# Kernel optimization log

Hardware: AMD Instinct MI355X
Metric: run time of the kernel (lower is better)

## Reference

```python
import jax, jax.numpy as jnp
import numpy as np

N_NODES = 100000
N_EDGES = 3200000
N_GRAPHS = 1000
IN_DIM = 10
HID = 20
N_CLASSES = 2
BN_EPS = 1e-5


def setup_inputs() -> dict:
    key = jax.random.key(0)
    ks = jax.random.split(key, 12)
    x = jax.random.normal(ks[0], (N_NODES, IN_DIM), dtype=jnp.float32)
    edge_index = jax.random.randint(ks[1], (2, N_EDGES), 0, N_NODES, dtype=jnp.int64)
    batch = jnp.sort(jax.random.randint(ks[2], (N_NODES,), 0, N_GRAPHS, dtype=jnp.int64))
    def lin(k, fan_in, fan_out):
        bound = 1.0 / np.sqrt(fan_in)
        kw, kb = jax.random.split(k)
        W = jax.random.uniform(kw, (fan_in, fan_out), jnp.float32, -bound, bound)
        b = jax.random.uniform(kb, (fan_out,), jnp.float32, -bound, bound)
        return W, b
    W1, b1 = lin(ks[3], IN_DIM, HID)
    W2, b2 = lin(ks[4], HID, HID)
    W3, b3 = lin(ks[5], HID, HID)
    fcW, fcb = lin(ks[6], HID, N_CLASSES)
    ones = jnp.ones((HID,), jnp.float32)
    zeros = jnp.zeros((HID,), jnp.float32)
    return {
        "x": x, "edge_index": edge_index, "batch": batch,
        "W1": W1, "b1": b1, "g1": ones, "beta1": zeros,
        "W2": W2, "b2": b2, "g2": ones, "beta2": zeros,
        "W3": W3, "b3": b3, "g3": ones, "beta3": zeros,
        "fcW": fcW, "fcb": fcb,
    }


def _gin_layer(h, src, dst, W, b, g, beta):
    # GIN aggregation: (1+eps)*x_i + sum_{j->i} x_j, eps = 0
    agg = jax.ops.segment_sum(h[src], dst, num_segments=N_NODES)  # [N, d]
    h = (h + agg) @ W + b                                          # MLP (single Linear)
    mu = jnp.mean(h, axis=0)                                       # BatchNorm (batch stats)
    var = jnp.mean(jnp.square(h - mu), axis=0)
    h = (h - mu) * jax.lax.rsqrt(var + BN_EPS) * g + beta
    return jax.nn.relu(h)                                          # dropout p=0 is identity


def reference(x, edge_index, batch, W1, b1, g1, beta1, W2, b2, g2, beta2,
              W3, b3, g3, beta3, fcW, fcb):
    src, dst = edge_index[0], edge_index[1]
    h = _gin_layer(x, src, dst, W1, b1, g1, beta1)
    h = _gin_layer(h, src, dst, W2, b2, g2, beta2)
    h = _gin_layer(h, src, dst, W3, b3, g3, beta3)
    graph_emb = jax.ops.segment_sum(h, batch, num_segments=N_GRAPHS)  # global add pool
    return graph_emb @ fcW + fcb
```

## Files before the change

### kernel.cpp

```cpp
#include <hip/hip_runtime.h>
#include <hip/hip_bf16.h>

#define N_NODES  100000
#define N_EDGES  3200000
#define N_GRAPHS 1000
#define IN_DIM   10
#define HID      20
#define BN_EPS   1e-5f

#define BSH   7
#define NB    ((N_NODES + 127) / 128)
#define FILL_BLOCKS 512
#define CHUNK ((N_EDGES + FILL_BLOCKS - 1) / FILL_BLOCKS)
#define MAXB  6144
#define NBG   ((N_NODES + 31) / 32)

__global__ __launch_bounds__(256) void hist_bucket(const int* __restrict__ dst,
                                                   int* __restrict__ gcnt) {
    __shared__ int cnt[NB];
    for (int i = threadIdx.x; i < NB; i += 256) cnt[i] = 0;
    __syncthreads();
    int e0 = blockIdx.x * CHUNK;
    int e1 = min(e0 + CHUNK, N_EDGES);
    for (int e = e0 + threadIdx.x; e < e1; e += 256)
        atomicAdd(&cnt[dst[e] >> BSH], 1);
    __syncthreads();
    for (int i = threadIdx.x; i < NB; i += 256)
        if (cnt[i]) atomicAdd(&gcnt[i], cnt[i]);
}

__global__ void scan_buckets(const int* __restrict__ gcnt,
                             int* __restrict__ off, int* __restrict__ cursor) {
    __shared__ int lds[1024];
    int t = threadIdx.x;
    int v = (t < NB) ? gcnt[t] : 0;
    int val = v;
    lds[t] = val; __syncthreads();
    for (int o = 1; o < 1024; o <<= 1) {
        int a = (t >= o) ? lds[t - o] : 0;
        __syncthreads();
        val += a; lds[t] = val;
        __syncthreads();
    }
    if (t < NB) { off[t] = val - v; cursor[t] = val - v; }
    if (t == 0) off[NB] = N_EDGES;
}

__global__ __launch_bounds__(256) void fill_bucket(const int* __restrict__ src,
                                                   const int* __restrict__ dst,
                                                   int* __restrict__ cursor,
                                                   unsigned* __restrict__ packed) {
    __shared__ int cnt[NB];
    __shared__ int base[NB];
    for (int i = threadIdx.x; i < NB; i += 256) cnt[i] = 0;
    __syncthreads();
    int e0 = blockIdx.x * CHUNK;
    int e1 = min(e0 + CHUNK, N_EDGES);
    for (int e = e0 + threadIdx.x; e < e1; e += 256)
        atomicAdd(&cnt[dst[e] >> BSH], 1);
    __syncthreads();
    for (int i = threadIdx.x; i < NB; i += 256) {
        int c = cnt[i];
        base[i] = c ? atomicAdd(&cursor[i], c) : 0;
        cnt[i] = 0;
    }
    __syncthreads();
    for (int e = e0 + threadIdx.x; e < e1; e += 256) {
        int d = dst[e];
        int b = d >> BSH;
        int lr = atomicAdd(&cnt[b], 1);
        packed[base[b] + lr] = (unsigned)src[e] | ((unsigned)(d & 127) << 24);
    }
}

__global__ __launch_bounds__(256) void sort_bucket(const unsigned* __restrict__ packed,
                                                   const int* __restrict__ off,
                                                   int* __restrict__ csr,
                                                   int* __restrict__ rp) {
    __shared__ unsigned ebuf[MAXB];
    __shared__ int cnt[256];
    __shared__ int cur[256];
    int b = blockIdx.x, t = threadIdx.x;
    int e0 = off[b], e1 = off[b + 1], m = e1 - e0;
    bool inl = (m <= MAXB);
    if (inl)
        for (int i = t; i < m; i += 256) ebuf[i] = packed[e0 + i];
    cnt[t] = 0;
    __syncthreads();
    for (int i = t; i < m; i += 256) {
        unsigned p = inl ? ebuf[i] : packed[e0 + i];
        atomicAdd(&cnt[p >> 24], 1);
    }
    __syncthreads();
    int v = cnt[t], val = v;
    cur[t] = val; __syncthreads();
    for (int o = 1; o < 256; o <<= 1) {
        int a = (t >= o) ? cur[t - o] : 0;
        __syncthreads();
        val += a; cur[t] = val;
        __syncthreads();
    }
    int excl = val - v;
    if (t < 128) {
        int node = b * 128 + t;
        if (node <= N_NODES) rp[node] = e0 + excl;
    }
    cur[t] = excl;
    __syncthreads();
    for (int i = t; i < m; i += 256) {
        unsigned p = inl ? ebuf[i] : packed[e0 + i];
        int l = p >> 24;
        int pos = atomicAdd(&cur[l], 1);
        csr[e0 + pos] = (int)(p & 0xFFFFFFu);
    }
}

template<int DIN, bool BN>
__global__ __launch_bounds__(256) void gather_mlp8(
        const float* __restrict__ h,
        const int* __restrict__ rp, const int* __restrict__ csr,
        const float* __restrict__ W,
        const float* __restrict__ bias,
        const float* __restrict__ ssin,
        float* __restrict__ hpre,
        float* __restrict__ partials)
{
    __shared__ float sW[DIN * HID];
    __shared__ float sb[HID];
    __shared__ float sss[2 * HID];
    __shared__ float red[4][2 * HID];
    int t = threadIdx.x;
    for (int i = t; i < DIN * HID; i += 256) sW[i] = W[i];
    if (t < HID) sb[t] = bias[t];
    if constexpr (BN) { if (t < 2 * HID) sss[t] = ssin[t]; }
    __syncthreads();

    int node = blockIdx.x * 32 + (t >> 3);
    int sub  = t & 7;
    float u[DIN];
#pragma unroll
    for (int k = 0; k < DIN; k++) u[k] = 0.0f;

    if (node < N_NODES) {
        int e0 = rp[node], e1 = rp[node + 1];
        if (sub == 0) {
            if constexpr (DIN == 20) {
                const float4* hv = (const float4*)(h + (size_t)node * 20);
#pragma unroll
                for (int q = 0; q < 5; q++) {
                    float4 a = hv[q];
                    float v0 = a.x, v1 = a.y, v2 = a.z, v3 = a.w;
                    if constexpr (BN) {
                        v0 = fmaxf(fmaf(v0, sss[4*q+0], sss[HID+4*q+0]), 0.f);
                        v1 = fmaxf(fmaf(v1, sss[4*q+1], sss[HID+4*q+1]), 0.f);
                        v2 = fmaxf(fmaf(v2, sss[4*q+2], sss[HID+4*q+2]), 0.f);
                        v3 = fmaxf(fmaf(v3, sss[4*q+3], sss[HID+4*q+3]), 0.f);
                    }
                    u[4*q] += v0; u[4*q+1] += v1; u[4*q+2] += v2; u[4*q+3] += v3;
                }
            } else {
                const float2* hv = (const float2*)(h + (size_t)node * DIN);
#pragma unroll
                for (int q = 0; q < 5; q++) {
                    float2 a = hv[q];
                    u[2*q] += a.x; u[2*q+1] += a.y;
                }
            }
        }
        int e = e0 + sub;
        for (; e + 8 < e1; e += 16) {
            int s0 = csr[e], s1 = csr[e + 8];
            if constexpr (DIN == 20) {
                const float4* a0 = (const float4*)(h + (size_t)s0 * 20);
                const float4* a1 = (const float4*)(h + (size_t)s1 * 20);
#pragma unroll
                for (int q = 0; q < 5; q++) {
                    float4 x0 = a0[q], x1 = a1[q];
                    if constexpr (BN) {
                        x0.x = fmaxf(fmaf(x0.x, sss[4*q+0], sss[HID+4*q+0]), 0.f);
                        x0.y = fmaxf(fmaf(x0.y, sss[4*q+1], sss[HID+4*q+1]), 0.f);
                        x0.z = fmaxf(fmaf(x0.z, sss[4*q+2], sss[HID+4*q+2]), 0.f);
                        x0.w = fmaxf(fmaf(x0.w, sss[4*q+3], sss[HID+4*q+3]), 0.f);
                        x1.x = fmaxf(fmaf(x1.x, sss[4*q+0], sss[HID+4*q+0]), 0.f);
                        x1.y = fmaxf(fmaf(x1.y, sss[4*q+1], sss[HID+4*q+1]), 0.f);
                        x1.z = fmaxf(fmaf(x1.z, sss[4*q+2], sss[HID+4*q+2]), 0.f);
                        x1.w = fmaxf(fmaf(x1.w, sss[4*q+3], sss[HID+4*q+3]), 0.f);
                    }
                    u[4*q]   += x0.x + x1.x;
                    u[4*q+1] += x0.y + x1.y;
                    u[4*q+2] += x0.z + x1.z;
                    u[4*q+3] += x0.w + x1.w;
                }
            } else {
                const float2* a0 = (const float2*)(h + (size_t)s0 * DIN);
                const float2* a1 = (const float2*)(h + (size_t)s1 * DIN);
#pragma unroll
                for (int q = 0; q < 5; q++) {
                    float2 x0 = a0[q], x1 = a1[q];
                    u[2*q]   += x0.x + x1.x;
                    u[2*q+1] += x0.y + x1.y;
                }
            }
        }
        for (; e < e1; e += 8) {
            int s0 = csr[e];
            if constexpr (DIN == 20) {
                const float4* a0 = (const float4*)(h + (size_t)s0 * 20);
#pragma unroll
                for (int q = 0; q < 5; q++) {
                    float4 x0 = a0[q];
                    if constexpr (BN) {
                        x0.x = fmaxf(fmaf(x0.x, sss[4*q+0], sss[HID+4*q+0]), 0.f);
                        x0.y = fmaxf(fmaf(x0.y, sss[4*q+1], sss[HID+4*q+1]), 0.f);
                        x0.z = fmaxf(fmaf(x0.z, sss[4*q+2], sss[HID+4*q+2]), 0.f);
                        x0.w = fmaxf(fmaf(x0.w, sss[4*q+3], sss[HID+4*q+3]), 0.f);
                    }
                    u[4*q] += x0.x; u[4*q+1] += x0.y; u[4*q+2] += x0.z; u[4*q+3] += x0.w;
                }
            } else {
                const float2* a0 = (const float2*)(h + (size_t)s0 * DIN);
#pragma unroll
                for (int q = 0; q < 5; q++) {
                    float2 x0 = a0[q];
                    u[2*q] += x0.x; u[2*q+1] += x0.y;
                }
            }
        }
    }

#pragma unroll
    for (int k = 0; k < DIN; k++) {
        u[k] += __shfl_xor(u[k], 1);
        u[k] += __shfl_xor(u[k], 2);
        u[k] += __shfl_xor(u[k], 4);
    }

    const int c0 = (sub & 3) * 5;
    float out[5];
#pragma unroll
    for (int j = 0; j < 5; j++) out[j] = sb[c0 + j];
#pragma unroll
    for (int k = 0; k < DIN; k++) {
        float uk = u[k];
#pragma unroll
        for (int j = 0; j < 5; j++)
            out[j] = fmaf(uk, sW[k * HID + c0 + j], out[j]);
    }
    bool live = (node < N_NODES) && (sub < 4);
    if (live) {
        float* op = hpre + (size_t)node * HID + c0;
#pragma unroll
        for (int j = 0; j < 5; j++) op[j] = out[j];
    }

    float msk = live ? 1.0f : 0.0f;
    float s1[5], s2[5];
#pragma unroll
    for (int j = 0; j < 5; j++) {
        float o = out[j] * msk;
        s1[j] = o; s2[j] = o * out[j];
    }
    for (int o = 8; o < 64; o <<= 1) {
#pragma unroll
        for (int j = 0; j < 5; j++) {
            s1[j] += __shfl_down(s1[j], o);
            s2[j] += __shfl_down(s2[j], o);
        }
    }
    int lane = t & 63, wave = t >> 6;
    if (lane < 4) {
#pragma unroll
        for (int j = 0; j < 5; j++) {
            red[wave][lane * 5 + j]       = s1[j];
            red[wave][HID + lane * 5 + j] = s2[j];
        }
    }
    __syncthreads();
    if (t < 2 * HID)
        partials[(size_t)t * NBG + blockIdx.x] =
            red[0][t] + red[1][t] + red[2][t] + red[3][t];
}

__global__ __launch_bounds__(256) void bn_prep(const float* __restrict__ partials,
                                               const float* __restrict__ g,
                                               const float* __restrict__ beta,
                                               float* __restrict__ ss) {
    int c = blockIdx.x, t = threadIdx.x;
    double a1 = 0.0, a2 = 0.0;
    for (int i = t; i < NBG; i += 256) {
        a1 += (double)partials[(size_t)c * NBG + i];
        a2 += (double)partials[(size_t)(c + HID) * NBG + i];
    }
    for (int o = 32; o; o >>= 1) {
        a1 += __shfl_down(a1, o);
        a2 += __shfl_down(a2, o);
    }
    __shared__ double r1[4], r2[4];
    int lane = t & 63, wave = t >> 6;
    if (lane == 0) { r1[wave] = a1; r2[wave] = a2; }
    __syncthreads();
    if (t == 0) {
        double su = r1[0] + r1[1] + r1[2] + r1[3];
        double sq = r2[0] + r2[1] + r2[2] + r2[3];
        double mu  = su / (double)N_NODES;
        double var = sq / (double)N_NODES - mu * mu;
        float sc = g[c] * (float)(1.0 / sqrt(var + (double)BN_EPS));
        ss[c]       = sc;
        ss[HID + c] = beta[c] - (float)mu * sc;
    }
}

__global__ void gptr_kernel(const int* __restrict__ batch, int* __restrict__ gptr) {
    int n = blockIdx.x * blockDim.x + threadIdx.x;
    if (n >= N_NODES) return;
    int g = batch[n];
    int gp = (n == 0) ? -1 : batch[n - 1];
    for (int q = gp + 1; q <= g; q++) gptr[q] = n;
    if (n == N_NODES - 1)
        for (int q = g + 1; q <= N_GRAPHS; q++) gptr[q] = N_NODES;
}

__global__ __launch_bounds__(256) void pool_fc(const float* __restrict__ h,
                                               const int* __restrict__ gptr,
                                               const float* __restrict__ ss,
                                               const float* __restrict__ fcW,
                                               const float* __restrict__ fcb,
                                               float* __restrict__ out) {
    __shared__ float red[12][HID];
    __shared__ float sss[2 * HID];
    __shared__ float pl[HID];
    int g = blockIdx.x, t = threadIdx.x;
    if (t < 2 * HID) sss[t] = ss[t];
    __syncthreads();
    int n0 = gptr[g], n1 = gptr[g + 1];
    if (t < 240) {
        int c = t % HID, grp = t / HID;
        float s = 0.0f;
        for (int n = n0 + grp; n < n1; n += 12) {
            float v = fmaf(h[(size_t)n * HID + c], sss[c], sss[HID + c]);
            s += v > 0.0f ? v : 0.0f;
        }
        red[grp][c] = s;
    }
    __syncthreads();
    if (t < HID) {
        float a = 0.0f;
#pragma unroll
        for (int q = 0; q < 12; q++) a += red[q][t];
        pl[t] = a;
    }
    __syncthreads();
    if (t < 2) {
        float o = fcb[t];
#pragma unroll
        for (int k = 0; k < HID; k++) o = fmaf(pl[k], fcW[k * 2 + t], o);
        out[g * 2 + t] = o;
    }
}

extern "C" void kernel_launch(void* const* d_in, const int* in_sizes, int n_in,
                              void* d_out, int out_size, void* d_ws, size_t ws_size,
                              hipStream_t stream) {
    const float* x     = (const float*)d_in[0];
    const int*   eidx  = (const int*)d_in[1];
    const int*   batch = (const int*)d_in[2];
    const float* W1 = (const float*)d_in[3];
    const float* b1 = (const float*)d_in[4];
    const float* g1 = (const float*)d_in[5];
    const float* be1 = (const float*)d_in[6];
    const float* W2 = (const float*)d_in[7];
    const float* b2 = (const float*)d_in[8];
    const float* g2 = (const float*)d_in[9];
    const float* be2 = (const float*)d_in[10];
    const float* W3 = (const float*)d_in[11];
    const float* b3 = (const float*)d_in[12];
    const float* g3 = (const float*)d_in[13];
    const float* be3 = (const float*)d_in[14];
    const float* fcW = (const float*)d_in[15];
    const float* fcb = (const float*)d_in[16];
    float* out = (float*)d_out;

    const int* src = eidx;
    const int* dst = eidx + N_EDGES;

    char* ws = (char*)d_ws;
    float* hA      = (float*)(ws + 0);
    float* hB      = (float*)(ws + 8000000);
    unsigned* packed = (unsigned*)(ws + 0);
    int*   csr     = (int*)(ws + 16000000);
    int*   rp      = (int*)(ws + 28800000);
    int*   off     = (int*)(ws + 29200128);
    int*   cursor  = (int*)(ws + 29203328);
    int*   gcnt    = (int*)(ws + 29206528);
    float* partials= (float*)(ws + 29209728);
    float* ss1     = (float*)(ws + 29709728);
    float* ss2     = (float*)(ws + 29709888);
    float* ss3     = (float*)(ws + 29710048);
    int*   gptr    = (int*)(ws + 29710208);

    const int BLK = 256;

    hipMemsetAsync(gcnt, 0, NB * sizeof(int), stream);
    hist_bucket<<<FILL_BLOCKS, BLK, 0, stream>>>(dst, gcnt);
    scan_buckets<<<1, 1024, 0, stream>>>(gcnt, off, cursor);
    fill_bucket<<<FILL_BLOCKS, BLK, 0, stream>>>(src, dst, cursor, packed);
    sort_bucket<<<NB, BLK, 0, stream>>>(packed, off, csr, rp);
    gptr_kernel<<<(N_NODES + BLK - 1) / BLK, BLK, 0, stream>>>(batch, gptr);

    gather_mlp8<IN_DIM, false><<<NBG, BLK, 0, stream>>>(x, rp, csr, W1, b1, ss1, hA, partials);
    bn_prep<<<HID, BLK, 0, stream>>>(partials, g1, be1, ss1);

    gather_mlp8<HID, true><<<NBG, BLK, 0, stream>>>(hA, rp, csr, W2, b2, ss1, hB, partials);
    bn_prep<<<HID, BLK, 0, stream>>>(partials, g2, be2, ss2);

    gather_mlp8<HID, true><<<NBG, BLK, 0, stream>>>(hB, rp, csr, W3, b3, ss2, hA, partials);
    bn_prep<<<HID, BLK, 0, stream>>>(partials, g3, be3, ss3);

    pool_fc<<<N_GRAPHS, BLK, 0, stream>>>(hA, gptr, ss3, fcW, fcb, out);
}
```

Baseline: 366.9 us.

## Merge histogram and fill into fixed-capacity buckets; unroll gather loads four-wide

Drops the separate histogram pass over the destination array. Edges now scatter straight into per-bucket regions of fixed capacity (CAP slots per 128-node bucket), with each block's destination chunk cached in LDS. The scan then runs on the final bucket counts, and the sort kernel reads each bucket from its fixed slot using 512 threads. The gather loop is unrolled to four independent row loads per iteration so more loads are in flight. The fixed capacity assumes no bucket receives more than CAP edges; a skewed degree distribution would overflow and corrupt memory.

```diff
diff --git a/kernel.cpp b/kernel.cpp
--- a/kernel.cpp
+++ b/kernel.cpp
@@ -10,30 +10,50 @@
 
 #define BSH   7
 #define NB    ((N_NODES + 127) / 128)
-#define FILL_BLOCKS 512
-#define CHUNK ((N_EDGES + FILL_BLOCKS - 1) / FILL_BLOCKS)
-#define MAXB  6144
+#define CAP   4608
+#define FB    512
+#define FT    512
+#define FCHUNK ((N_EDGES + FB - 1) / FB)
 #define NBG   ((N_NODES + 31) / 32)
 
-__global__ __launch_bounds__(256) void hist_bucket(const int* __restrict__ dst,
-                                                   int* __restrict__ gcnt) {
+__global__ __launch_bounds__(FT) void fill_direct(const int* __restrict__ src,
+                                                  const int* __restrict__ dst,
+                                                  int* __restrict__ bcur,
+                                                  unsigned* __restrict__ packed) {
+    __shared__ int sdst[FCHUNK];
     __shared__ int cnt[NB];
-    for (int i = threadIdx.x; i < NB; i += 256) cnt[i] = 0;
-    __syncthreads();
-    int e0 = blockIdx.x * CHUNK;
-    int e1 = min(e0 + CHUNK, N_EDGES);
-    for (int e = e0 + threadIdx.x; e < e1; e += 256)
-        atomicAdd(&cnt[dst[e] >> BSH], 1);
-    __syncthreads();
-    for (int i = threadIdx.x; i < NB; i += 256)
-        if (cnt[i]) atomicAdd(&gcnt[i], cnt[i]);
-}
-
-__global__ void scan_buckets(const int* __restrict__ gcnt,
-                             int* __restrict__ off, int* __restrict__ cursor) {
+    __shared__ int base[NB];
+    int t = threadIdx.x;
+    for (int i = t; i < NB; i += FT) cnt[i] = 0;
+    __syncthreads();
+    int e0 = blockIdx.x * FCHUNK;
+    int e1 = min(e0 + FCHUNK, N_EDGES);
+    int m = e1 - e0;
+    for (int i = t; i < m; i += FT) {
+        int d = dst[e0 + i];
+        sdst[i] = d;
+        atomicAdd(&cnt[d >> BSH], 1);
+    }
+    __syncthreads();
+    for (int i = t; i < NB; i += FT) {
+        int c = cnt[i];
+        base[i] = c ? atomicAdd(&bcur[i], c) : 0;
+        cnt[i] = 0;
+    }
+    __syncthreads();
+    for (int i = t; i < m; i += FT) {
+        int d = sdst[i];
+        int b = d >> BSH;
+        int r = atomicAdd(&cnt[b], 1);
+        packed[(size_t)b * CAP + base[b] + r] =
+            (unsigned)src[e0 + i] | ((unsigned)(d & 127) << 24);
+    }
+}
+
+__global__ void scan_buckets(const int* __restrict__ bcur, int* __restrict__ off) {
     __shared__ int lds[1024];
     int t = threadIdx.x;
-    int v = (t < NB) ? gcnt[t] : 0;
+    int v = (t < NB) ? bcur[t] : 0;
     int val = v;
     lds[t] = val; __syncthreads();
     for (int o = 1; o < 1024; o <<= 1) {
@@ -42,76 +62,47 @@
         val += a; lds[t] = val;
         __syncthreads();
     }
-    if (t < NB) { off[t] = val - v; cursor[t] = val - v; }
+    if (t < NB) off[t] = val - v;
     if (t == 0) off[NB] = N_EDGES;
 }
 
-__global__ __launch_bounds__(256) void fill_bucket(const int* __restrict__ src,
-                                                   const int* __restrict__ dst,
-                                                   int* __restrict__ cursor,
-                                                   unsigned* __restrict__ packed) {
-    __shared__ int cnt[NB];
-    __shared__ int base[NB];
-    for (int i = threadIdx.x; i < NB; i += 256) cnt[i] = 0;
-    __syncthreads();
-    int e0 = blockIdx.x * CHUNK;
-    int e1 = min(e0 + CHUNK, N_EDGES);
-    for (int e = e0 + threadIdx.x; e < e1; e += 256)
-        atomicAdd(&cnt[dst[e] >> BSH], 1);
-    __syncthreads();
-    for (int i = threadIdx.x; i < NB; i += 256) {
-        int c = cnt[i];
-        base[i] = c ? atomicAdd(&cursor[i], c) : 0;
-        cnt[i] = 0;
-    }
-    __syncthreads();
-    for (int e = e0 + threadIdx.x; e < e1; e += 256) {
-        int d = dst[e];
-        int b = d >> BSH;
-        int lr = atomicAdd(&cnt[b], 1);
-        packed[base[b] + lr] = (unsigned)src[e] | ((unsigned)(d & 127) << 24);
-    }
-}
-
-__global__ __launch_bounds__(256) void sort_bucket(const unsigned* __restrict__ packed,
+__global__ __launch_bounds__(512) void sort_bucket(const unsigned* __restrict__ packed,
+                                                   const int* __restrict__ bcnt,
                                                    const int* __restrict__ off,
                                                    int* __restrict__ csr,
                                                    int* __restrict__ rp) {
-    __shared__ unsigned ebuf[MAXB];
-    __shared__ int cnt[256];
-    __shared__ int cur[256];
+    __shared__ unsigned ebuf[CAP];
+    __shared__ int cnt[128];
+    __shared__ int cur[128];
     int b = blockIdx.x, t = threadIdx.x;
-    int e0 = off[b], e1 = off[b + 1], m = e1 - e0;
-    bool inl = (m <= MAXB);
-    if (inl)
-        for (int i = t; i < m; i += 256) ebuf[i] = packed[e0 + i];
-    cnt[t] = 0;
-    __syncthreads();
-    for (int i = t; i < m; i += 256) {
-        unsigned p = inl ? ebuf[i] : packed[e0 + i];
-        atomicAdd(&cnt[p >> 24], 1);
-    }
-    __syncthreads();
-    int v = cnt[t], val = v;
-    cur[t] = val; __syncthreads();
-    for (int o = 1; o < 256; o <<= 1) {
-        int a = (t >= o) ? cur[t - o] : 0;
+    int m = bcnt[b];
+    int o = off[b];
+    const unsigned* pb = packed + (size_t)b * CAP;
+    for (int i = t; i < m; i += 512) ebuf[i] = pb[i];
+    if (t < 128) cnt[t] = 0;
+    __syncthreads();
+    for (int i = t; i < m; i += 512) atomicAdd(&cnt[ebuf[i] >> 24], 1);
+    __syncthreads();
+    int v = 0, val = 0;
+    if (t < 128) { v = cnt[t]; val = v; cur[t] = val; }
+    __syncthreads();
+    for (int ofs = 1; ofs < 128; ofs <<= 1) {
+        int add = (t < 128 && t >= ofs) ? cur[t - ofs] : 0;
         __syncthreads();
-        val += a; cur[t] = val;
+        if (t < 128) { val += add; cur[t] = val; }
         __syncthreads();
     }
-    int excl = val - v;
     if (t < 128) {
         int node = b * 128 + t;
-        if (node <= N_NODES) rp[node] = e0 + excl;
-    }
-    cur[t] = excl;
-    __syncthreads();
-    for (int i = t; i < m; i += 256) {
-        unsigned p = inl ? ebuf[i] : packed[e0 + i];
+        if (node <= N_NODES) rp[node] = o + (val - v);
+        cur[t] = val - v;
+    }
+    __syncthreads();
+    for (int i = t; i < m; i += 512) {
+        unsigned p = ebuf[i];
         int l = p >> 24;
         int pos = atomicAdd(&cur[l], 1);
-        csr[e0 + pos] = (int)(p & 0xFFFFFFu);
+        csr[o + pos] = (int)(p & 0xFFFFFFu);
     }
 }
 
@@ -141,23 +132,24 @@
 #pragma unroll
     for (int k = 0; k < DIN; k++) u[k] = 0.0f;
 
+    auto acc4 = [&](float4 a, int q) {
+        float v0 = a.x, v1 = a.y, v2 = a.z, v3 = a.w;
+        if constexpr (BN) {
+            v0 = fmaxf(fmaf(v0, sss[4*q+0], sss[HID+4*q+0]), 0.f);
+            v1 = fmaxf(fmaf(v1, sss[4*q+1], sss[HID+4*q+1]), 0.f);
+            v2 = fmaxf(fmaf(v2, sss[4*q+2], sss[HID+4*q+2]), 0.f);
+            v3 = fmaxf(fmaf(v3, sss[4*q+3], sss[HID+4*q+3]), 0.f);
+        }
+        u[4*q] += v0; u[4*q+1] += v1; u[4*q+2] += v2; u[4*q+3] += v3;
+    };
+
     if (node < N_NODES) {
         int e0 = rp[node], e1 = rp[node + 1];
         if (sub == 0) {
             if constexpr (DIN == 20) {
                 const float4* hv = (const float4*)(h + (size_t)node * 20);
 #pragma unroll
-                for (int q = 0; q < 5; q++) {
-                    float4 a = hv[q];
-                    float v0 = a.x, v1 = a.y, v2 = a.z, v3 = a.w;
-                    if constexpr (BN) {
-                        v0 = fmaxf(fmaf(v0, sss[4*q+0], sss[HID+4*q+0]), 0.f);
-                        v1 = fmaxf(fmaf(v1, sss[4*q+1], sss[HID+4*q+1]), 0.f);
-                        v2 = fmaxf(fmaf(v2, sss[4*q+2], sss[HID+4*q+2]), 0.f);
-                        v3 = fmaxf(fmaf(v3, sss[4*q+3], sss[HID+4*q+3]), 0.f);
-                    }
-                    u[4*q] += v0; u[4*q+1] += v1; u[4*q+2] += v2; u[4*q+3] += v3;
-                }
+                for (int q = 0; q < 5; q++) acc4(hv[q], q);
             } else {
                 const float2* hv = (const float2*)(h + (size_t)node * DIN);
 #pragma unroll
@@ -168,57 +160,68 @@
             }
         }
         int e = e0 + sub;
-        for (; e + 8 < e1; e += 16) {
-            int s0 = csr[e], s1 = csr[e + 8];
-            if constexpr (DIN == 20) {
+        if constexpr (DIN == 20) {
+            for (; e + 24 < e1; e += 32) {
+                int s0 = csr[e], s1 = csr[e + 8], s2 = csr[e + 16], s3 = csr[e + 24];
                 const float4* a0 = (const float4*)(h + (size_t)s0 * 20);
                 const float4* a1 = (const float4*)(h + (size_t)s1 * 20);
+                const float4* a2 = (const float4*)(h + (size_t)s2 * 20);
+                const float4* a3 = (const float4*)(h + (size_t)s3 * 20);
+                float4 r0[5], r1[5], r2[5], r3[5];
+#pragma unroll
+                for (int q = 0; q < 5; q++) r0[q] = a0[q];
+#pragma unroll
+                for (int q = 0; q < 5; q++) r1[q] = a1[q];
+#pragma unroll
+                for (int q = 0; q < 5; q++) r2[q] = a2[q];
+#pragma unroll
+                for (int q = 0; q < 5; q++) r3[q] = a3[q];
 #pragma unroll
                 for (int q = 0; q < 5; q++) {
-                    float4 x0 = a0[q], x1 = a1[q];
-                    if constexpr (BN) {
-                        x0.x = fmaxf(fmaf(x0.x, sss[4*q+0], sss[HID+4*q+0]), 0.f);
-                        x0.y = fmaxf(fmaf(x0.y, sss[4*q+1], sss[HID+4*q+1]), 0.f);
-                        x0.z = fmaxf(fmaf(x0.z, sss[4*q+2], sss[HID+4*q+2]), 0.f);
-                        x0.w = fmaxf(fmaf(x0.w, sss[4*q+3], sss[HID+4*q+3]), 0.f);
-                        x1.x = fmaxf(fmaf(x1.x, sss[4*q+0], sss[HID+4*q+0]), 0.f);
-                        x1.y = fmaxf(fmaf(x1.y, sss[4*q+1], sss[HID+4*q+1]), 0.f);
-                        x1.z = fmaxf(fmaf(x1.z, sss[4*q+2], sss[HID+4*q+2]), 0.f);
-                        x1.w = fmaxf(fmaf(x1.w, sss[4*q+3], sss[HID+4*q+3]), 0.f);
-                    }
-                    u[4*q]   += x0.x + x1.x;
-                    u[4*q+1] += x0.y + x1.y;
-                    u[4*q+2] += x0.z + x1.z;
-                    u[4*q+3] += x0.w + x1.w;
+                    acc4(r0[q], q); acc4(r1[q], q); acc4(r2[q], q); acc4(r3[q], q);
                 }
-            } else {
+            }
+            for (; e + 8 < e1; e += 16) {
+                int s0 = csr[e], s1 = csr[e + 8];
+                const float4* a0 = (const float4*)(h + (size_t)s0 * 20);
+                const float4* a1 = (const float4*)(h + (size_t)s1 * 20);
+                float4 r0[5], r1[5];
+#pragma unroll
+                for (int q = 0; q < 5; q++) r0[q] = a0[q];
+#pragma unroll
+                for (int q = 0; q < 5; q++) r1[q] = a1[q];
+#pragma unroll
+                for (int q = 0; q < 5; q++) { acc4(r0[q], q); acc4(r1[q], q); }
+            }
+            if (e < e1) {
+                const float4* a0 = (const float4*)(h + (size_t)csr[e] * 20);
+#pragma unroll
+                for (int q = 0; q < 5; q++) acc4(a0[q], q);
+            }
+        } else {
+            for (; e + 24 < e1; e += 32) {
+                int s0 = csr[e], s1 = csr[e + 8], s2 = csr[e + 16], s3 = csr[e + 24];
                 const float2* a0 = (const float2*)(h + (size_t)s0 * DIN);
                 const float2* a1 = (const float2*)(h + (size_t)s1 * DIN);
+                const float2* a2 = (const float2*)(h + (size_t)s2 * DIN);
+                const float2* a3 = (const float2*)(h + (size_t)s3 * DIN);
+                float2 r0[5], r1[5], r2[5], r3[5];
+#pragma unroll
+                for (int q = 0; q < 5; q++) r0[q] = a0[q];
+#pragma unroll
+                for (int q = 0; q < 5; q++) r1[q] = a1[q];
+#pragma unroll
+                for (int q = 0; q < 5; q++) r2[q] = a2[q];
+#pragma unroll
+                for (int q = 0; q < 5; q++) r3[q] = a3[q];
 #pragma unroll
                 for (int q = 0; q < 5; q++) {
-                    float2 x0 = a0[q], x1 = a1[q];
-                    u[2*q]   += x0.x + x1.x;
-                    u[2*q+1] += x0.y + x1.y;
+                    u[2*q]   += r0[q].x + r1[q].x + r2[q].x + r3[q].x;
+                    u[2*q+1] += r0[q].y + r1[q].y + r2[q].y + r3[q].y;
                 }
             }
-        }
-        for (; e < e1; e += 8) {
-            int s0 = csr[e];
-            if constexpr (DIN == 20) {
-                const float4* a0 = (const float4*)(h + (size_t)s0 * 20);
-#pragma unroll
-                for (int q = 0; q < 5; q++) {
-                    float4 x0 = a0[q];
-                    if constexpr (BN) {
-                        x0.x = fmaxf(fmaf(x0.x, sss[4*q+0], sss[HID+4*q+0]), 0.f);
-                        x0.y = fmaxf(fmaf(x0.y, sss[4*q+1], sss[HID+4*q+1]), 0.f);
-                        x0.z = fmaxf(fmaf(x0.z, sss[4*q+2], sss[HID+4*q+2]), 0.f);
-                        x0.w = fmaxf(fmaf(x0.w, sss[4*q+3], sss[HID+4*q+3]), 0.f);
-                    }
-                    u[4*q] += x0.x; u[4*q+1] += x0.y; u[4*q+2] += x0.z; u[4*q+3] += x0.w;
-                }
-            } else {
-                const float2* a0 = (const float2*)(h + (size_t)s0 * DIN);
+            for (; e < e1; e += 8) {
+                const float2* a0 = (const float2*)(h + (size_t)csr[e] * DIN);
 #pragma unroll
                 for (int q = 0; q < 5; q++) {
                     float2 x0 = a0[q];
@@ -390,8 +393,7 @@
     int*   csr     = (int*)(ws + 16000000);
     int*   rp      = (int*)(ws + 28800000);
     int*   off     = (int*)(ws + 29200128);
-    int*   cursor  = (int*)(ws + 29203328);
-    int*   gcnt    = (int*)(ws + 29206528);
+    int*   bcur    = (int*)(ws + 29203328);
     float* partials= (float*)(ws + 29209728);
     float* ss1     = (float*)(ws + 29709728);
     float* ss2     = (float*)(ws + 29709888);
@@ -400,11 +402,10 @@
 
     const int BLK = 256;
 
-    hipMemsetAsync(gcnt, 0, NB * sizeof(int), stream);
-    hist_bucket<<<FILL_BLOCKS, BLK, 0, stream>>>(dst, gcnt);
-    scan_buckets<<<1, 1024, 0, stream>>>(gcnt, off, cursor);
-    fill_bucket<<<FILL_BLOCKS, BLK, 0, stream>>>(src, dst, cursor, packed);
-    sort_bucket<<<NB, BLK, 0, stream>>>(packed, off, csr, rp);
+    hipMemsetAsync(bcur, 0, NB * sizeof(int), stream);
+    fill_direct<<<FB, FT, 0, stream>>>(src, dst, bcur, packed);
+    scan_buckets<<<1, 1024, 0, stream>>>(bcur, off);
+    sort_bucket<<<NB, 512, 0, stream>>>(packed, bcur, off, csr, rp);
     gptr_kernel<<<(N_NODES + BLK - 1) / BLK, BLK, 0, stream>>>(batch, gptr);
 
     gather_mlp8<IN_DIM, false><<<NBG, BLK, 0, stream>>>(x, rp, csr, W1, b1, ss1, hA, partials);
```

Measured after the change: 376.2 us. +2.5%, slower.
